# Kernel tuning notes

Hardware: AMD Instinct MI355X
Metric: run time of the kernel (lower is better)

The kernel has to match this reference:

```python
import jax, jax.numpy as jnp
import numpy as np

D_MODEL = 512  # = sub_length = seq_length (last axis of x)


def make_overlap_mask(S, n, m):
    # Faithful to MultiHeadSelfAttentiondis.create_mask:
    # True where 0.5 <= overlap_ratio < 1, or i == j. (The ratio>=1 elif branch is dead code.)
    d = np.abs(np.arange(S)[:, None] - np.arange(S)[None, :])
    overlap = np.maximum(0, m - d * n)
    ratio = overlap / float(m)
    mask = ((ratio >= 0.5) & (ratio < 1.0)) | (d == 0)
    return jnp.asarray(mask)


def setup_inputs() -> dict:
    key = jax.random.key(0)
    k1, k2, k3 = jax.random.split(key, 3)
    B, D, S, L = 16, 8, 256, D_MODEL
    x = jax.random.normal(k1, (B, D, S, L), dtype=jnp.float32)
    # nn.Linear(d_model, 3*d_model): weight [3L, L], bias [3L]
    Wqkv = jax.random.normal(k2, (3 * L, L), dtype=jnp.float32) / np.sqrt(L)
    bqkv = jax.random.normal(k3, (3 * L,), dtype=jnp.float32) * 0.01
    return {"x": x, "Wqkv": Wqkv, "bqkv": bqkv, "n": 256}


def reference(x, Wqkv, bqkv, n):
    B, D, S, L = x.shape
    mask = make_overlap_mask(S, n, L)  # [S, S] bool, static
    # Shared QKV projection, batched over all channels at once (replaces the per-dim loop)
    qkv = jnp.einsum('bdsl,fl->bdsf', x, Wqkv) + bqkv  # [B, D, S, 3L]
    q, k, v = jnp.split(qkv, 3, axis=-1)               # each [B, D, S, L]
    scores = jnp.einsum('bdsl,bdtl->bdst', q, k) / jnp.sqrt(jnp.float32(L))
    attn = jax.nn.softmax(scores, axis=-1)             # [B, D, S, S]
    # masked_fill(mask, 0) happens AFTER softmax in the original
    attn = jnp.where(mask[None, None], 0.0, attn)
    out = jnp.einsum('bdst,bdtl->bdsl', attn, v)       # [B, D, S, L]
    output = out.reshape(B, D * S, L)
    # Block-diagonal attention matrix: block d is attn[:, d]
    eyeD = jnp.eye(D, dtype=attn.dtype)
    big = eyeD[None, :, None, :, None] * attn[:, :, :, None, :]  # [B, D, S, D, S]
    output_matrix_attn = big.reshape(B, D * S, D * S)
    return output, output_matrix_attn
```

## Files before the change

### kernel.cpp

```cpp
#include <hip/hip_runtime.h>
#include <hip/hip_bf16.h>
#include <cstdint>


typedef unsigned short u16;
typedef short bf16x8 __attribute__((ext_vector_type(8)));
typedef float f32x4 __attribute__((ext_vector_type(4)));

__device__ __forceinline__ u16 f2bf(float f) {
    union { float f; unsigned int u; } v; v.f = f;
    unsigned int r = v.u + 0x7FFF + ((v.u >> 16) & 1);
    return (u16)(r >> 16);
}

__device__ __forceinline__ void gload16(const u16* g, u16* l) {
    __builtin_amdgcn_global_load_lds(
        (const __attribute__((address_space(1))) unsigned int*)g,
        (__attribute__((address_space(3))) unsigned int*)l, 16, 0, 0);
}

__device__ __forceinline__ f32x4 mfma16(bf16x8 a, bf16x8 b, f32x4 c) {
    return __builtin_amdgcn_mfma_f32_16x16x32_bf16(a, b, c, 0, 0, 0);
}

__global__ __launch_bounds__(256) void cast_bf16(const float* __restrict__ x,
                                                 const float* __restrict__ w,
                                                 u16* __restrict__ xb,
                                                 u16* __restrict__ wb) {
    const size_t NX = 16777216 / 8, NW = 786432 / 8;
    size_t i = (size_t)blockIdx.x * 256 + threadIdx.x;
    const float* src; u16* dst; size_t e;
    if (i < NX)            { src = x; dst = xb; e = i; }
    else if (i < NX + NW)  { src = w; dst = wb; e = i - NX; }
    else return;
    const float4 a = *(const float4*)&src[e * 8];
    const float4 b = *(const float4*)&src[e * 8 + 4];
    u16 o[8] = { f2bf(a.x), f2bf(a.y), f2bf(a.z), f2bf(a.w),
                 f2bf(b.x), f2bf(b.y), f2bf(b.z), f2bf(b.w) };
    *(uint4*)&dst[e * 8] = *(const uint4*)o;
}

__global__ __launch_bounds__(256, 2) void qkv_gemm(const u16* __restrict__ xb,
                                                   const u16* __restrict__ wb,
                                                   const float* __restrict__ bias,
                                                   u16* __restrict__ qb,
                                                   u16* __restrict__ kb,
                                                   u16* __restrict__ vb) {
    __shared__ __align__(16) u16 sA[8 * 512];
    __shared__ __align__(16) u16 sB[16 * 512];
    const int tid = threadIdx.x, lane = tid & 63, w = tid >> 6;
    const int lr = lane & 15, lh = lane >> 4;
    const int f0 = blockIdx.x * 256, m0 = blockIdx.y * 128;
    const int wm = w & 1, wf = w >> 1;

    f32x4 acc[4][8];
#pragma unroll
    for (int i = 0; i < 4; ++i)
#pragma unroll
        for (int j = 0; j < 8; ++j) acc[i][j] = (f32x4){0.f, 0.f, 0.f, 0.f};

#pragma unroll 1
    for (int k0 = 0; k0 < 512; k0 += 32) {
#pragma unroll
        for (int i = 0; i < 6; ++i) {
            const int j = w * 6 + i;
            if (j < 8) {
                gload16(xb + (size_t)(m0 + j * 16 + lr) * 512 + k0 + lh * 8,
                        &sA[j * 512]);
            } else {
                const int jb = j - 8;
                gload16(wb + (size_t)(f0 + jb * 16 + lr) * 512 + k0 + lh * 8,
                        &sB[jb * 512]);
            }
        }
        __syncthreads();
        bf16x8 af[4], bf[8];
#pragma unroll
        for (int mt = 0; mt < 4; ++mt)
            af[mt] = *(const bf16x8*)&sA[(wm * 4 + mt) * 512 + lane * 8];
#pragma unroll
        for (int ft = 0; ft < 8; ++ft)
            bf[ft] = *(const bf16x8*)&sB[(wf * 8 + ft) * 512 + lane * 8];
#pragma unroll
        for (int mt = 0; mt < 4; ++mt)
#pragma unroll
            for (int ft = 0; ft < 8; ++ft)
                acc[mt][ft] = mfma16(af[mt], bf[ft], acc[mt][ft]);
        __syncthreads();
    }

    u16* patch = &sA[w * 1024];
    const int bdq = m0 >> 8;
    float bv[8];
#pragma unroll
    for (int ft = 0; ft < 8; ++ft) bv[ft] = bias[f0 + wf * 128 + ft * 16 + lr];

    if (f0 < 1024) {
        u16* dstb = (f0 < 512) ? qb : kb;
        const int mtileg = ((m0 & 255) >> 4) + wm * 4;
        const int kbase = ((f0 & 511) + wf * 128) >> 5;
#pragma unroll
        for (int mt = 0; mt < 4; ++mt)
#pragma unroll
            for (int ftp = 0; ftp < 4; ++ftp) {
#pragma unroll
                for (int h = 0; h < 2; ++h) {
                    const int ft = ftp * 2 + h;
                    const f32x4 a = acc[mt][ft];
#pragma unroll
                    for (int r = 0; r < 4; ++r)
                        patch[(lh * 4 + r) * 40 + h * 16 + lr] = f2bf(a[r] + bv[ft]);
                }
                asm volatile("s_waitcnt lgkmcnt(0)" ::: "memory");
                bf16x8 frag = *(const bf16x8*)&patch[lr * 40 + lh * 8];
                u16* dst = dstb +
                    ((size_t)(bdq * 16 + mtileg + mt) * 16 + (kbase + ftp)) * 512 +
                    lane * 8;
                *(bf16x8*)dst = frag;
            }
    } else {
        const int nbase = ((f0 - 1024) >> 4) + wf * 8;
        const int tbase = ((m0 & 255) >> 5) + wm * 2;
#pragma unroll
        for (int ft = 0; ft < 8; ++ft)
#pragma unroll
            for (int mtp = 0; mtp < 2; ++mtp) {
#pragma unroll
                for (int h = 0; h < 2; ++h) {
                    const f32x4 a = acc[mtp * 2 + h][ft];
#pragma unroll
                    for (int r = 0; r < 4; ++r)
                        patch[lr * 40 + h * 16 + lh * 4 + r] = f2bf(a[r] + bv[ft]);
                }
                asm volatile("s_waitcnt lgkmcnt(0)" ::: "memory");
                bf16x8 frag = *(const bf16x8*)&patch[lr * 40 + lh * 8];
                u16* dst = vb +
                    ((size_t)(bdq * 32 + nbase + ft) * 8 + (tbase + mtp)) * 512 +
                    lane * 8;
                *(bf16x8*)dst = frag;
            }
    }
}

__global__ __launch_bounds__(256, 2) void attn_kernel(const u16* __restrict__ qb,
                                                      const u16* __restrict__ kb,
                                                      const u16* __restrict__ vb,
                                                      const int* __restrict__ n_ptr,
                                                      float* __restrict__ out,
                                                      float* __restrict__ outmat) {
    __shared__ __align__(16) u16 sQ[4 * 512];
    __shared__ __align__(16) u16 sK[16 * 512];
    __shared__ __align__(16) u16 sP[8 * 4 * 512];
    __shared__ float sStat[64][2];

    const int tid = threadIdx.x, lane = tid & 63, w = tid >> 6;
    const int lr = lane & 15, lh = lane >> 4;
    const int r0 = blockIdx.x * 64, bd = blockIdx.y;
    const int n = *n_ptr;
    const int wm = w & 1, wt = w >> 1;
    const int b_ = bd >> 3, dd = bd & 7;
    float* zbase = &outmat[(size_t)b_ * 4194304 + (size_t)(dd * 256 + r0) * 2048];
    const float4 f4z = make_float4(0.f, 0.f, 0.f, 0.f);

    f32x4 acc[2][8];
#pragma unroll
    for (int i = 0; i < 2; ++i)
#pragma unroll
        for (int j = 0; j < 8; ++j) acc[i][j] = (f32x4){0.f, 0.f, 0.f, 0.f};

#pragma unroll 1
    for (int k0 = 0; k0 < 512; k0 += 32) {
        const int kc = k0 >> 5;
#pragma unroll
        for (int i = 0; i < 5; ++i) {
            const int j = w * 5 + i;
            if (j < 4) {
                gload16(qb + ((size_t)(bd * 16 + blockIdx.x * 4 + j) * 16 + kc) * 512 +
                        lane * 8, &sQ[j * 512]);
            } else {
                const int jb = j - 4;
                gload16(kb + ((size_t)(bd * 16 + jb) * 16 + kc) * 512 + lane * 8,
                        &sK[jb * 512]);
            }
        }
#pragma unroll
        for (int u = 0; u < 8; ++u) {
            const int idx = (kc * 8 + u) * 256 + tid;
            const int row = idx >> 9, c4 = idx & 511;
            if ((c4 >> 6) != dd)
                *(float4*)&zbase[(size_t)row * 2048 + c4 * 4] = f4z;
        }
        __syncthreads();
        bf16x8 af[2], bf[8];
#pragma unroll
        for (int mt = 0; mt < 2; ++mt)
            af[mt] = *(const bf16x8*)&sQ[(wm * 2 + mt) * 512 + lane * 8];
#pragma unroll
        for (int jt = 0; jt < 8; ++jt)
            bf[jt] = *(const bf16x8*)&sK[(wt * 8 + jt) * 512 + lane * 8];
#pragma unroll
        for (int mt = 0; mt < 2; ++mt)
#pragma unroll
            for (int jt = 0; jt < 8; ++jt)
                acc[mt][jt] = mfma16(af[mt], bf[jt], acc[mt][jt]);
        __syncthreads();
    }

    const float scale = 0.044194173824159216f;
#pragma unroll
    for (int i = 0; i < 2; ++i)
#pragma unroll
        for (int j = 0; j < 8; ++j) acc[i][j] *= scale;

    float rmax[2][4], rinv[2][4];
#pragma unroll
    for (int i = 0; i < 2; ++i)
#pragma unroll
        for (int r = 0; r < 4; ++r) {
            float v = -1e30f;
#pragma unroll
            for (int j = 0; j < 8; ++j) v = fmaxf(v, acc[i][j][r]);
            v = fmaxf(v, __shfl_xor(v, 1));
            v = fmaxf(v, __shfl_xor(v, 2));
            v = fmaxf(v, __shfl_xor(v, 4));
            v = fmaxf(v, __shfl_xor(v, 8));
            if (lr == 0) sStat[wm * 32 + i * 16 + lh * 4 + r][wt] = v;
        }
    __syncthreads();
#pragma unroll
    for (int i = 0; i < 2; ++i)
#pragma unroll
        for (int r = 0; r < 4; ++r) {
            const int m = wm * 32 + i * 16 + lh * 4 + r;
            rmax[i][r] = fmaxf(sStat[m][0], sStat[m][1]);
        }
    __syncthreads();
#pragma unroll
    for (int i = 0; i < 2; ++i)
#pragma unroll
        for (int r = 0; r < 4; ++r) {
            float s = 0.f;
#pragma unroll
            for (int j = 0; j < 8; ++j) {
                const float p = __expf(acc[i][j][r] - rmax[i][r]);
                acc[i][j][r] = p;
                s += p;
            }
            s += __shfl_xor(s, 1);
            s += __shfl_xor(s, 2);
            s += __shfl_xor(s, 4);
            s += __shfl_xor(s, 8);
            if (lr == 0) sStat[wm * 32 + i * 16 + lh * 4 + r][wt] = s;
        }
    __syncthreads();
#pragma unroll
    for (int i = 0; i < 2; ++i)
#pragma unroll
        for (int r = 0; r < 4; ++r) {
            const int m = wm * 32 + i * 16 + lh * 4 + r;
            rinv[i][r] = 1.0f / (sStat[m][0] + sStat[m][1]);
        }

#pragma unroll
    for (int i = 0; i < 2; ++i)
#pragma unroll
        for (int r = 0; r < 4; ++r) {
            const int m_loc = wm * 32 + i * 16 + lh * 4 + r;
            const int ig = r0 + m_loc;
            float* orow = &outmat[(size_t)b_ * 4194304 +
                                  (size_t)(dd * 256 + ig) * 2048 + dd * 256];
#pragma unroll
            for (int j = 0; j < 8; ++j) {
                const int t = wt * 128 + j * 16 + lr;
                float a = acc[i][j][r] * rinv[i][r];
                const int d = (ig > t) ? (ig - t) : (t - ig);
                int ov = 512 - d * n; if (ov < 0) ov = 0;
                if (d == 0 || ((2 * ov >= 512) && (ov < 512))) a = 0.f;
                orow[t] = a;
                sP[((t >> 5) * 4 + (m_loc >> 4)) * 512 +
                   (((t & 31) >> 3) * 16 + (m_loc & 15)) * 8 + (t & 7)] = f2bf(a);
            }
        }
    __syncthreads();

#pragma unroll 1
    for (int nc = 0; nc < 2; ++nc) {
#pragma unroll
        for (int i = 0; i < 2; ++i)
#pragma unroll
            for (int j = 0; j < 8; ++j) acc[i][j] = (f32x4){0.f, 0.f, 0.f, 0.f};
#pragma unroll 1
        for (int t0 = 0; t0 < 256; t0 += 32) {
            const int tc = t0 >> 5;
#pragma unroll
            for (int i = 0; i < 4; ++i) {
                const int nt = w * 4 + i;
                gload16(vb + ((size_t)(bd * 32 + nc * 16 + nt) * 8 + tc) * 512 +
                        lane * 8, &sK[nt * 512]);
            }
            __syncthreads();
            bf16x8 af[2], bf[8];
#pragma unroll
            for (int mt = 0; mt < 2; ++mt)
                af[mt] = *(const bf16x8*)&sP[(tc * 4 + wm * 2 + mt) * 512 + lane * 8];
#pragma unroll
            for (int jt = 0; jt < 8; ++jt)
                bf[jt] = *(const bf16x8*)&sK[(wt * 8 + jt) * 512 + lane * 8];
#pragma unroll
            for (int mt = 0; mt < 2; ++mt)
#pragma unroll
                for (int jt = 0; jt < 8; ++jt)
                    acc[mt][jt] = mfma16(af[mt], bf[jt], acc[mt][jt]);
            __syncthreads();
        }
#pragma unroll
        for (int mt = 0; mt < 2; ++mt)
#pragma unroll
            for (int jt = 0; jt < 8; ++jt) {
                const int ng = nc * 256 + wt * 128 + jt * 16 + lr;
#pragma unroll
                for (int r = 0; r < 4; ++r) {
                    const int m_loc = wm * 32 + mt * 16 + lh * 4 + r;
                    out[((size_t)bd * 256 + r0 + m_loc) * 512 + ng] = acc[mt][jt][r];
                }
            }
    }
}

extern "C" void kernel_launch(void* const* d_in, const int* in_sizes, int n_in,
                              void* d_out, int out_size, void* d_ws, size_t ws_size,
                              hipStream_t stream) {
    (void)in_sizes; (void)n_in; (void)out_size; (void)ws_size;
    const float* x     = (const float*)d_in[0];
    const float* Wqkv  = (const float*)d_in[1];
    const float* bqkv  = (const float*)d_in[2];
    const int*   n_ptr = (const int*)d_in[3];

    float* out    = (float*)d_out;
    float* outmat = out + (size_t)16 * 2048 * 512;

    u16* xb = (u16*)d_ws;
    u16* wb = xb + 16777216;
    u16* qb = wb + 786432;
    u16* kb = qb + 16777216;
    u16* vb = kb + 16777216;

    cast_bf16<<<8576, 256, 0, stream>>>(x, Wqkv, xb, wb);

    dim3 g1(6, 256);
    qkv_gemm<<<g1, 256, 0, stream>>>(xb, wb, bqkv, qb, kb, vb);

    dim3 g2(4, 128);
    attn_kernel<<<g2, 256, 0, stream>>>(qb, kb, vb, n_ptr, out, outmat);
}
```

Baseline: 515.5 us.

## Double-buffer attention LDS tiles and remap blocks across XCDs

```diff
diff --git a/kernel.cpp b/kernel.cpp
--- a/kernel.cpp
+++ b/kernel.cpp
@@ -50,7 +50,11 @@
     __shared__ __align__(16) u16 sB[16 * 512];
     const int tid = threadIdx.x, lane = tid & 63, w = tid >> 6;
     const int lr = lane & 15, lh = lane >> 4;
-    const int f0 = blockIdx.x * 256, m0 = blockIdx.y * 128;
+    const int bfl = blockIdx.x;
+    const int work = (bfl & 7) * 192 + (bfl >> 3);
+    const int mb = work / 6;
+    const int fb = work - mb * 6;
+    const int f0 = fb * 256, m0 = mb * 128;
     const int wm = w & 1, wf = w >> 1;
 
     f32x4 acc[4][8];
@@ -148,14 +152,17 @@
                                                       const int* __restrict__ n_ptr,
                                                       float* __restrict__ out,
                                                       float* __restrict__ outmat) {
-    __shared__ __align__(16) u16 sQ[4 * 512];
-    __shared__ __align__(16) u16 sK[16 * 512];
+    __shared__ __align__(16) u16 sQ[2][4 * 512];
+    __shared__ __align__(16) u16 sK[2][16 * 512];
     __shared__ __align__(16) u16 sP[8 * 4 * 512];
     __shared__ float sStat[64][2];
 
     const int tid = threadIdx.x, lane = tid & 63, w = tid >> 6;
     const int lr = lane & 15, lh = lane >> 4;
-    const int r0 = blockIdx.x * 64, bd = blockIdx.y;
+    const int bfl = blockIdx.x;
+    const int work = (bfl & 7) * 64 + (bfl >> 3);
+    const int bd = work >> 2, rblk = work & 3;
+    const int r0 = rblk * 64;
     const int n = *n_ptr;
     const int wm = w & 1, wt = w >> 1;
     const int b_ = bd >> 3, dd = bd & 7;
@@ -168,42 +175,66 @@
 #pragma unroll
         for (int j = 0; j < 8; ++j) acc[i][j] = (f32x4){0.f, 0.f, 0.f, 0.f};
 
-#pragma unroll 1
-    for (int k0 = 0; k0 < 512; k0 += 32) {
-        const int kc = k0 >> 5;
+    {
 #pragma unroll
         for (int i = 0; i < 5; ++i) {
             const int j = w * 5 + i;
-            if (j < 4) {
-                gload16(qb + ((size_t)(bd * 16 + blockIdx.x * 4 + j) * 16 + kc) * 512 +
-                        lane * 8, &sQ[j * 512]);
-            } else {
-                const int jb = j - 4;
-                gload16(kb + ((size_t)(bd * 16 + jb) * 16 + kc) * 512 + lane * 8,
-                        &sK[jb * 512]);
-            }
-        }
+            if (j < 4)
+                gload16(qb + ((size_t)(bd * 16 + rblk * 4 + j) * 16 + 0) * 512 +
+                        lane * 8, &sQ[0][j * 512]);
+            else
+                gload16(kb + ((size_t)(bd * 16 + (j - 4)) * 16 + 0) * 512 + lane * 8,
+                        &sK[0][(j - 4) * 512]);
+        }
+        __builtin_amdgcn_sched_barrier(0);
 #pragma unroll
         for (int u = 0; u < 8; ++u) {
-            const int idx = (kc * 8 + u) * 256 + tid;
-            const int row = idx >> 9, c4 = idx & 511;
-            if ((c4 >> 6) != dd)
-                *(float4*)&zbase[(size_t)row * 2048 + c4 * 4] = f4z;
-        }
-        __syncthreads();
-        bf16x8 af[2], bf[8];
-#pragma unroll
-        for (int mt = 0; mt < 2; ++mt)
-            af[mt] = *(const bf16x8*)&sQ[(wm * 2 + mt) * 512 + lane * 8];
+            const int idx = u * 256 + tid;
+            *(float4*)&zbase[(size_t)(idx >> 9) * 2048 + (idx & 511) * 4] = f4z;
+        }
+        asm volatile("s_waitcnt vmcnt(8)" ::: "memory");
+        __builtin_amdgcn_s_barrier();
+        __builtin_amdgcn_sched_barrier(0);
+    }
+
+#pragma unroll 1
+    for (int kc = 0; kc < 16; ++kc) {
+        const int cur = kc & 1;
+        if (kc < 15) {
+#pragma unroll
+            for (int i = 0; i < 5; ++i) {
+                const int j = w * 5 + i;
+                if (j < 4)
+                    gload16(qb + ((size_t)(bd * 16 + rblk * 4 + j) * 16 + (kc + 1)) * 512 +
+                            lane * 8, &sQ[cur ^ 1][j * 512]);
+                else
+                    gload16(kb + ((size_t)(bd * 16 + (j - 4)) * 16 + (kc + 1)) * 512 +
+                            lane * 8, &sK[cur ^ 1][(j - 4) * 512]);
+            }
+            __builtin_amdgcn_sched_barrier(0);
+#pragma unroll
+            for (int u = 0; u < 8; ++u) {
+                const int idx = ((kc + 1) * 8 + u) * 256 + tid;
+                *(float4*)&zbase[(size_t)(idx >> 9) * 2048 + (idx & 511) * 4] = f4z;
+            }
+        }
+        bf16x8 af[2], bfr[8];
+#pragma unroll
+        for (int mt = 0; mt < 2; ++mt)
+            af[mt] = *(const bf16x8*)&sQ[cur][(wm * 2 + mt) * 512 + lane * 8];
 #pragma unroll
         for (int jt = 0; jt < 8; ++jt)
-            bf[jt] = *(const bf16x8*)&sK[(wt * 8 + jt) * 512 + lane * 8];
+            bfr[jt] = *(const bf16x8*)&sK[cur][(wt * 8 + jt) * 512 + lane * 8];
 #pragma unroll
         for (int mt = 0; mt < 2; ++mt)
 #pragma unroll
             for (int jt = 0; jt < 8; ++jt)
-                acc[mt][jt] = mfma16(af[mt], bf[jt], acc[mt][jt]);
-        __syncthreads();
+                acc[mt][jt] = mfma16(af[mt], bfr[jt], acc[mt][jt]);
+        if (kc < 15) {
+            asm volatile("s_waitcnt vmcnt(8)" ::: "memory");
+            __builtin_amdgcn_s_barrier();
+            __builtin_amdgcn_sched_barrier(0);
+        }
     }
 
     const float scale = 0.044194173824159216f;
@@ -253,6 +284,14 @@
             if (lr == 0) sStat[wm * 32 + i * 16 + lh * 4 + r][wt] = s;
         }
     __syncthreads();
+
+#pragma unroll
+    for (int i = 0; i < 4; ++i) {
+        const int nt = w * 4 + i;
+        gload16(vb + ((size_t)(bd * 32 + nt) * 8 + 0) * 512 + lane * 8,
+                &sK[0][nt * 512]);
+    }
+
 #pragma unroll
     for (int i = 0; i < 2; ++i)
 #pragma unroll
@@ -283,48 +322,88 @@
         }
     __syncthreads();
 
+    f32x4 accB[2][8];
+#pragma unroll
+    for (int i = 0; i < 2; ++i)
+#pragma unroll
+        for (int j = 0; j < 8; ++j) acc[i][j] = (f32x4){0.f, 0.f, 0.f, 0.f};
+
 #pragma unroll 1
-    for (int nc = 0; nc < 2; ++nc) {
-#pragma unroll
-        for (int i = 0; i < 2; ++i)
-#pragma unroll
-            for (int j = 0; j < 8; ++j) acc[i][j] = (f32x4){0.f, 0.f, 0.f, 0.f};
+    for (int step = 0; step < 8; ++step) {
+        const int cur = step & 1;
+        const int ns = step + 1;
+#pragma unroll
+        for (int i = 0; i < 4; ++i) {
+            const int nt = w * 4 + i;
+            gload16(vb + ((size_t)(bd * 32 + (ns >> 3) * 16 + nt) * 8 + (ns & 7)) * 512 +
+                    lane * 8, &sK[cur ^ 1][nt * 512]);
+        }
+        bf16x8 af[2], bfr[8];
+#pragma unroll
+        for (int mt = 0; mt < 2; ++mt)
+            af[mt] = *(const bf16x8*)&sP[(step * 4 + wm * 2 + mt) * 512 + lane * 8];
+#pragma unroll
+        for (int jt = 0; jt < 8; ++jt)
+            bfr[jt] = *(const bf16x8*)&sK[cur][(wt * 8 + jt) * 512 + lane * 8];
+#pragma unroll
+        for (int mt = 0; mt < 2; ++mt)
+#pragma unroll
+            for (int jt = 0; jt < 8; ++jt)
+                acc[mt][jt] = mfma16(af[mt], bfr[jt], acc[mt][jt]);
+        asm volatile("s_waitcnt vmcnt(0)" ::: "memory");
+        __builtin_amdgcn_s_barrier();
+        __builtin_amdgcn_sched_barrier(0);
+    }
+
+#pragma unroll
+    for (int i = 0; i < 2; ++i)
+#pragma unroll
+        for (int j = 0; j < 8; ++j) accB[i][j] = (f32x4){0.f, 0.f, 0.f, 0.f};
+
 #pragma unroll 1
-        for (int t0 = 0; t0 < 256; t0 += 32) {
-            const int tc = t0 >> 5;
+    for (int step = 8; step < 16; ++step) {
+        const int cur = step & 1, tc = step & 7;
+        if (step < 15) {
+            const int ns = step + 1;
 #pragma unroll
             for (int i = 0; i < 4; ++i) {
                 const int nt = w * 4 + i;
-                gload16(vb + ((size_t)(bd * 32 + nc * 16 + nt) * 8 + tc) * 512 +
-                        lane * 8, &sK[nt * 512]);
-            }
-            __syncthreads();
-            bf16x8 af[2], bf[8];
-#pragma unroll
-            for (int mt = 0; mt < 2; ++mt)
-                af[mt] = *(const bf16x8*)&sP[(tc * 4 + wm * 2 + mt) * 512 + lane * 8];
+                gload16(vb + ((size_t)(bd * 32 + 16 + nt) * 8 + (ns & 7)) * 512 +
+                        lane * 8, &sK[cur ^ 1][nt * 512]);
+            }
+        }
+        bf16x8 af[2], bfr[8];
+#pragma unroll
+        for (int mt = 0; mt < 2; ++mt)
+            af[mt] = *(const bf16x8*)&sP[(tc * 4 + wm * 2 + mt) * 512 + lane * 8];
+#pragma unroll
+        for (int jt = 0; jt < 8; ++jt)
+            bfr[jt] = *(const bf16x8*)&sK[cur][(wt * 8 + jt) * 512 + lane * 8];
+#pragma unroll
+        for (int mt = 0; mt < 2; ++mt)
 #pragma unroll
             for (int jt = 0; jt < 8; ++jt)
-                bf[jt] = *(const bf16x8*)&sK[(wt * 8 + jt) * 512 + lane * 8];
-#pragma unroll
-            for (int mt = 0; mt < 2; ++mt)
-#pragma unroll
-                for (int jt = 0; jt < 8; ++jt)
-                    acc[mt][jt] = mfma16(af[mt], bf[jt], acc[mt][jt]);
-            __syncthreads();
-        }
-#pragma unroll
-        for (int mt = 0; mt < 2; ++mt)
-#pragma unroll
-            for (int jt = 0; jt < 8; ++jt) {
-                const int ng = nc * 256 + wt * 128 + jt * 16 + lr;
-#pragma unroll
-                for (int r = 0; r < 4; ++r) {
-                    const int m_loc = wm * 32 + mt * 16 + lh * 4 + r;
-                    out[((size_t)bd * 256 + r0 + m_loc) * 512 + ng] = acc[mt][jt][r];
-                }
-            }
-    }
+                accB[mt][jt] = mfma16(af[mt], bfr[jt], accB[mt][jt]);
+        if (step < 15) {
+            asm volatile("s_waitcnt vmcnt(0)" ::: "memory");
+            __builtin_amdgcn_s_barrier();
+            __builtin_amdgcn_sched_barrier(0);
+        }
+    }
+
+#pragma unroll
+    for (int mt = 0; mt < 2; ++mt)
+#pragma unroll
+        for (int jt = 0; jt < 8; ++jt) {
+            const int ng = wt * 128 + jt * 16 + lr;
+#pragma unroll
+            for (int r = 0; r < 4; ++r) {
+                const int m_loc = wm * 32 + mt * 16 + lh * 4 + r;
+                float* orow = &out[((size_t)bd * 256 + r0 + m_loc) * 512];
+                orow[ng] = acc[mt][jt][r];
+                orow[256 + ng] = accB[mt][jt][r];
+            }
+        }
 }
 
 extern "C" void kernel_launch(void* const* d_in, const int* in_sizes, int n_in,
@@ -347,9 +426,7 @@
 
     cast_bf16<<<8576, 256, 0, stream>>>(x, Wqkv, xb, wb);
 
-    dim3 g1(6, 256);
-    qkv_gemm<<<g1, 256, 0, stream>>>(xb, wb, bqkv, qb, kb, vb);
-
-    dim3 g2(4, 128);
-    attn_kernel<<<g2, 256, 0, stream>>>(qb, kb, vb, n_ptr, out, outmat);
-}
+    qkv_gemm<<<1536, 256, 0, stream>>>(xb, wb, bqkv, qb, kb, vb);
+
+    attn_kernel<<<512, 256, 0, stream>>>(qb, kb, vb, n_ptr, out, outmat);
+}
```

Measured after the change: 512.2 us. Within noise of the previous version (-0.6%).

## Load Q/K/V fragments directly from global, add XCD-aware block remap and nontemporal stores

Applied to the files above, without the earlier changes.

```diff
diff --git a/kernel.cpp b/kernel.cpp
--- a/kernel.cpp
+++ b/kernel.cpp
@@ -33,10 +33,10 @@
     if (i < NX)            { src = x; dst = xb; e = i; }
     else if (i < NX + NW)  { src = w; dst = wb; e = i - NX; }
     else return;
-    const float4 a = *(const float4*)&src[e * 8];
-    const float4 b = *(const float4*)&src[e * 8 + 4];
-    u16 o[8] = { f2bf(a.x), f2bf(a.y), f2bf(a.z), f2bf(a.w),
-                 f2bf(b.x), f2bf(b.y), f2bf(b.z), f2bf(b.w) };
+    const f32x4 a = __builtin_nontemporal_load((const f32x4*)&src[e * 8]);
+    const f32x4 b = __builtin_nontemporal_load((const f32x4*)&src[e * 8 + 4]);
+    u16 o[8] = { f2bf(a[0]), f2bf(a[1]), f2bf(a[2]), f2bf(a[3]),
+                 f2bf(b[0]), f2bf(b[1]), f2bf(b[2]), f2bf(b[3]) };
     *(uint4*)&dst[e * 8] = *(const uint4*)o;
 }
 
@@ -50,7 +50,11 @@
     __shared__ __align__(16) u16 sB[16 * 512];
     const int tid = threadIdx.x, lane = tid & 63, w = tid >> 6;
     const int lr = lane & 15, lh = lane >> 4;
-    const int f0 = blockIdx.x * 256, m0 = blockIdx.y * 128;
+    const int bfl = blockIdx.x;
+    const int work = (bfl & 7) * 192 + (bfl >> 3);
+    const int mb = work / 6;
+    const int fb = work - mb * 6;
+    const int f0 = fb * 256, m0 = mb * 128;
     const int wm = w & 1, wf = w >> 1;
 
     f32x4 acc[4][8];
@@ -116,7 +120,7 @@
                 u16* dst = dstb +
                     ((size_t)(bdq * 16 + mtileg + mt) * 16 + (kbase + ftp)) * 512 +
                     lane * 8;
-                *(bf16x8*)dst = frag;
+                __builtin_nontemporal_store(frag, (bf16x8*)dst);
             }
     } else {
         const int nbase = ((f0 - 1024) >> 4) + wf * 8;
@@ -137,7 +141,7 @@
                 u16* dst = vb +
                     ((size_t)(bdq * 32 + nbase + ft) * 8 + (tbase + mtp)) * 512 +
                     lane * 8;
-                *(bf16x8*)dst = frag;
+                __builtin_nontemporal_store(frag, (bf16x8*)dst);
             }
     }
 }
@@ -148,19 +152,19 @@
                                                       const int* __restrict__ n_ptr,
                                                       float* __restrict__ out,
                                                       float* __restrict__ outmat) {
-    __shared__ __align__(16) u16 sQ[4 * 512];
-    __shared__ __align__(16) u16 sK[16 * 512];
     __shared__ __align__(16) u16 sP[8 * 4 * 512];
     __shared__ float sStat[64][2];
 
     const int tid = threadIdx.x, lane = tid & 63, w = tid >> 6;
     const int lr = lane & 15, lh = lane >> 4;
-    const int r0 = blockIdx.x * 64, bd = blockIdx.y;
+    const int bfl = blockIdx.x;
+    const int work = (bfl & 7) * 64 + (bfl >> 3);
+    const int bd = work >> 2, rblk = work & 3;
+    const int r0 = rblk * 64;
     const int n = *n_ptr;
     const int wm = w & 1, wt = w >> 1;
     const int b_ = bd >> 3, dd = bd & 7;
     float* zbase = &outmat[(size_t)b_ * 4194304 + (size_t)(dd * 256 + r0) * 2048];
-    const float4 f4z = make_float4(0.f, 0.f, 0.f, 0.f);
 
     f32x4 acc[2][8];
 #pragma unroll
@@ -168,42 +172,30 @@
 #pragma unroll
         for (int j = 0; j < 8; ++j) acc[i][j] = (f32x4){0.f, 0.f, 0.f, 0.f};
 
-#pragma unroll 1
-    for (int k0 = 0; k0 < 512; k0 += 32) {
-        const int kc = k0 >> 5;
-#pragma unroll
-        for (int i = 0; i < 5; ++i) {
-            const int j = w * 5 + i;
-            if (j < 4) {
-                gload16(qb + ((size_t)(bd * 16 + blockIdx.x * 4 + j) * 16 + kc) * 512 +
-                        lane * 8, &sQ[j * 512]);
-            } else {
-                const int jb = j - 4;
-                gload16(kb + ((size_t)(bd * 16 + jb) * 16 + kc) * 512 + lane * 8,
-                        &sK[jb * 512]);
-            }
-        }
+    const u16* qbase = qb + ((size_t)(bd * 16 + rblk * 4 + wm * 2) * 16) * 512 + lane * 8;
+    const u16* kbase = kb + ((size_t)(bd * 16 + wt * 8) * 16) * 512 + lane * 8;
+
+#pragma unroll 2
+    for (int kc = 0; kc < 16; ++kc) {
+        bf16x8 af[2], bfr[8];
+#pragma unroll
+        for (int mt = 0; mt < 2; ++mt)
+            af[mt] = *(const bf16x8*)(qbase + (size_t)(mt * 16 + kc) * 512);
+#pragma unroll
+        for (int jt = 0; jt < 8; ++jt)
+            bfr[jt] = *(const bf16x8*)(kbase + (size_t)(jt * 16 + kc) * 512);
 #pragma unroll
         for (int u = 0; u < 8; ++u) {
             const int idx = (kc * 8 + u) * 256 + tid;
-            const int row = idx >> 9, c4 = idx & 511;
-            if ((c4 >> 6) != dd)
-                *(float4*)&zbase[(size_t)row * 2048 + c4 * 4] = f4z;
-        }
-        __syncthreads();
-        bf16x8 af[2], bf[8];
-#pragma unroll
-        for (int mt = 0; mt < 2; ++mt)
-            af[mt] = *(const bf16x8*)&sQ[(wm * 2 + mt) * 512 + lane * 8];
-#pragma unroll
-        for (int jt = 0; jt < 8; ++jt)
-            bf[jt] = *(const bf16x8*)&sK[(wt * 8 + jt) * 512 + lane * 8];
+            const f32x4 z = (f32x4){0.f, 0.f, 0.f, 0.f};
+            __builtin_nontemporal_store(
+                z, (f32x4*)&zbase[(size_t)(idx >> 9) * 2048 + (idx & 511) * 4]);
+        }
 #pragma unroll
         for (int mt = 0; mt < 2; ++mt)
 #pragma unroll
             for (int jt = 0; jt < 8; ++jt)
-                acc[mt][jt] = mfma16(af[mt], bf[jt], acc[mt][jt]);
-        __syncthreads();
+                acc[mt][jt] = mfma16(af[mt], bfr[jt], acc[mt][jt]);
     }
 
     const float scale = 0.044194173824159216f;
@@ -276,55 +268,81 @@
                 const int d = (ig > t) ? (ig - t) : (t - ig);
                 int ov = 512 - d * n; if (ov < 0) ov = 0;
                 if (d == 0 || ((2 * ov >= 512) && (ov < 512))) a = 0.f;
-                orow[t] = a;
+                __builtin_nontemporal_store(a, &orow[t]);
                 sP[((t >> 5) * 4 + (m_loc >> 4)) * 512 +
                    (((t & 31) >> 3) * 16 + (m_loc & 15)) * 8 + (t & 7)] = f2bf(a);
             }
         }
     __syncthreads();
 
-#pragma unroll 1
-    for (int nc = 0; nc < 2; ++nc) {
-#pragma unroll
-        for (int i = 0; i < 2; ++i)
-#pragma unroll
-            for (int j = 0; j < 8; ++j) acc[i][j] = (f32x4){0.f, 0.f, 0.f, 0.f};
-#pragma unroll 1
-        for (int t0 = 0; t0 < 256; t0 += 32) {
-            const int tc = t0 >> 5;
-#pragma unroll
-            for (int i = 0; i < 4; ++i) {
-                const int nt = w * 4 + i;
-                gload16(vb + ((size_t)(bd * 32 + nc * 16 + nt) * 8 + tc) * 512 +
-                        lane * 8, &sK[nt * 512]);
-            }
-            __syncthreads();
-            bf16x8 af[2], bf[8];
-#pragma unroll
-            for (int mt = 0; mt < 2; ++mt)
-                af[mt] = *(const bf16x8*)&sP[(tc * 4 + wm * 2 + mt) * 512 + lane * 8];
+    const u16* vbase = vb + ((size_t)(bd * 32 + wt * 8) * 8) * 512 + lane * 8;
+
+#pragma unroll
+    for (int i = 0; i < 2; ++i)
+#pragma unroll
+        for (int j = 0; j < 8; ++j) acc[i][j] = (f32x4){0.f, 0.f, 0.f, 0.f};
+#pragma unroll 2
+    for (int tc = 0; tc < 8; ++tc) {
+        bf16x8 af[2], bfr[8];
+#pragma unroll
+        for (int mt = 0; mt < 2; ++mt)
+            af[mt] = *(const bf16x8*)&sP[(tc * 4 + wm * 2 + mt) * 512 + lane * 8];
+#pragma unroll
+        for (int jt = 0; jt < 8; ++jt)
+            bfr[jt] = *(const bf16x8*)(vbase + (size_t)(jt * 8 + tc) * 512);
+#pragma unroll
+        for (int mt = 0; mt < 2; ++mt)
 #pragma unroll
             for (int jt = 0; jt < 8; ++jt)
-                bf[jt] = *(const bf16x8*)&sK[(wt * 8 + jt) * 512 + lane * 8];
-#pragma unroll
-            for (int mt = 0; mt < 2; ++mt)
-#pragma unroll
-                for (int jt = 0; jt < 8; ++jt)
-                    acc[mt][jt] = mfma16(af[mt], bf[jt], acc[mt][jt]);
-            __syncthreads();
-        }
-#pragma unroll
-        for (int mt = 0; mt < 2; ++mt)
-#pragma unroll
-            for (int jt = 0; jt < 8; ++jt) {
-                const int ng = nc * 256 + wt * 128 + jt * 16 + lr;
-#pragma unroll
-                for (int r = 0; r < 4; ++r) {
-                    const int m_loc = wm * 32 + mt * 16 + lh * 4 + r;
-                    out[((size_t)bd * 256 + r0 + m_loc) * 512 + ng] = acc[mt][jt][r];
-                }
-            }
-    }
+                acc[mt][jt] = mfma16(af[mt], bfr[jt], acc[mt][jt]);
+    }
+#pragma unroll
+    for (int mt = 0; mt < 2; ++mt)
+#pragma unroll
+        for (int jt = 0; jt < 8; ++jt) {
+            const int ng = wt * 128 + jt * 16 + lr;
+#pragma unroll
+            for (int r = 0; r < 4; ++r) {
+                const int m_loc = wm * 32 + mt * 16 + lh * 4 + r;
+                __builtin_nontemporal_store(
+                    acc[mt][jt][r],
+                    &out[((size_t)bd * 256 + r0 + m_loc) * 512 + ng]);
+            }
+        }
+
+#pragma unroll
+    for (int i = 0; i < 2; ++i)
+#pragma unroll
+        for (int j = 0; j < 8; ++j) acc[i][j] = (f32x4){0.f, 0.f, 0.f, 0.f};
+    const u16* vbase1 = vbase + (size_t)16 * 8 * 512;
+#pragma unroll 2
+    for (int tc = 0; tc < 8; ++tc) {
+        bf16x8 af[2], bfr[8];
+#pragma unroll
+        for (int mt = 0; mt < 2; ++mt)
+            af[mt] = *(const bf16x8*)&sP[(tc * 4 + wm * 2 + mt) * 512 + lane * 8];
+#pragma unroll
+        for (int jt = 0; jt < 8; ++jt)
+            bfr[jt] = *(const bf16x8*)(vbase1 + (size_t)(jt * 8 + tc) * 512);
+#pragma unroll
+        for (int mt = 0; mt < 2; ++mt)
+#pragma unroll
+            for (int jt = 0; jt < 8; ++jt)
+                acc[mt][jt] = mfma16(af[mt], bfr[jt], acc[mt][jt]);
+    }
+#pragma unroll
+    for (int mt = 0; mt < 2; ++mt)
+#pragma unroll
+        for (int jt = 0; jt < 8; ++jt) {
+            const int ng = 256 + wt * 128 + jt * 16 + lr;
+#pragma unroll
+            for (int r = 0; r < 4; ++r) {
+                const int m_loc = wm * 32 + mt * 16 + lh * 4 + r;
+                __builtin_nontemporal_store(
+                    acc[mt][jt][r],
+                    &out[((size_t)bd * 256 + r0 + m_loc) * 512 + ng]);
+            }
+        }
 }
 
 extern "C" void kernel_launch(void* const* d_in, const int* in_sizes, int n_in,
@@ -347,9 +365,7 @@
 
     cast_bf16<<<8576, 256, 0, stream>>>(x, Wqkv, xb, wb);
 
-    dim3 g1(6, 256);
-    qkv_gemm<<<g1, 256, 0, stream>>>(xb, wb, bqkv, qb, kb, vb);
-
-    dim3 g2(4, 128);
-    attn_kernel<<<g2, 256, 0, stream>>>(qb, kb, vb, n_ptr, out, outmat);
-}
+    qkv_gemm<<<1536, 256, 0, stream>>>(xb, wb, bqkv, qb, kb, vb);
+
+    attn_kernel<<<512, 256, 0, stream>>>(qb, kb, vb, n_ptr, out, outmat);
+}
```

Measured after the change: 543.0 us. 5.3% more time.
